# Performance work log

Hardware: AMD Instinct MI355X
Metric: run time of the kernel (lower is better)

Reference implementation:

```python
import jax, jax.numpy as jnp
import numpy as np

B, L = 16, 128
E, A = 34, 36          # num_events, num_arguments
V, D, H = 30000, 300, 256


def setup_inputs() -> dict:
    key = jax.random.key(0)
    ks = jax.random.split(key, 14)
    s = 0.08
    n = lambda k, shape: jax.random.normal(k, shape, jnp.float32) * s
    return {
        "input_ids": jax.random.randint(ks[0], (B, L), 0, V),
        "emb": n(ks[1], (V, D)),
        "Wih_f": n(ks[2], (4 * H, D)), "Whh_f": n(ks[3], (4 * H, H)),
        "bih_f": n(ks[4], (4 * H,)), "bhh_f": n(ks[5], (4 * H,)),
        "Wih_b": n(ks[6], (4 * H, D)), "Whh_b": n(ks[7], (4 * H, H)),
        "bih_b": n(ks[8], (4 * H,)), "bhh_b": n(ks[9], (4 * H,)),
        "We": n(ks[10], (E, 2 * H + E - 1)), "be": n(ks[11], (E,)),
        "Wa": n(ks[12], (A, 4 * H + A - 1 + E - 1)), "ba": n(ks[13], (A,)),
    }


def _lstm(x, Wih, Whh, bih, bhh):
    # x: [L, B, D] -> outputs [L, B, H]; PyTorch gate order i, f, g, o
    Bsz = x.shape[1]
    Hh = Whh.shape[1]
    b = bih + bhh

    def step(carry, xt):
        h, c = carry
        z = xt @ Wih.T + h @ Whh.T + b
        i, f, g, o = jnp.split(z, 4, axis=-1)
        c = jax.nn.sigmoid(f) * c + jax.nn.sigmoid(i) * jnp.tanh(g)
        h = jax.nn.sigmoid(o) * jnp.tanh(c)
        return (h, c), h

    h0 = jnp.zeros((Bsz, Hh), x.dtype)
    _, hs = jax.lax.scan(step, (h0, h0), x)
    return hs


def _forward(input_ids, emb, Wih_f, Whh_f, bih_f, bhh_f, Wih_b, Whh_b, bih_b, bhh_b, We, be, Wa, ba):
    Bsz, Ll = input_ids.shape
    x = emb[input_ids]                       # [B, L, D]
    xt = jnp.transpose(x, (1, 0, 2))         # [L, B, D]
    hf = _lstm(xt, Wih_f, Whh_f, bih_f, bhh_f)
    hb = _lstm(xt[::-1], Wih_b, Whh_b, bih_b, bhh_b)[::-1]
    hs = jnp.concatenate([hf, hb], axis=-1)  # [L, B, 2H]
    hidden = jnp.transpose(hs, (1, 0, 2))    # [B, L, 2H]

    ev_ids = jnp.arange(E - 1)
    ar_ids = jnp.arange(A - 1)
    g_trg0 = jnp.zeros((Bsz, E - 1), jnp.int32)
    g_trg_arg0 = jnp.zeros((Bsz, Ll, E - 1), jnp.int32)
    g_arg0 = jnp.zeros((Bsz, Ll, A - 1), jnp.int32)

    def step(carry, ht):                     # ht: [B, 2H] at position i
        g_trg, g_trg_arg, g_arg = carry
        ev_in = jnp.concatenate([ht, g_trg.astype(ht.dtype)], axis=1)
        ev_logit = ev_in @ We.T + be                       # [B, E]
        ev_pred = jnp.argmax(ev_logit, axis=-1)            # [B]
        trig = jnp.broadcast_to(ht[:, None, :], (Bsz, Ll, ht.shape[-1]))
        arg_in = jnp.concatenate(
            [hidden, trig, g_arg.astype(ht.dtype), g_trg_arg.astype(ht.dtype)], axis=2)
        arg_logits = arg_in @ Wa.T + ba                    # [B, L, A]
        arg_pred = jnp.argmax(arg_logits, axis=-1)         # [B, L]

        has_ev = ev_pred > 0
        # update_g_trg: g_trg[b, ev_pred[b]-1] = 1 where ev_pred>0
        g_trg = jnp.where(has_ev[:, None] & (ev_ids[None, :] == (ev_pred - 1)[:, None]), 1, g_trg)
        # update_g_trg_arg: column ev_pred-1 set to 1 where arg_pred>0
        cond_ta = (has_ev[:, None, None] & (arg_pred > 0)[:, :, None]
                   & (ev_ids[None, None, :] == (ev_pred - 1)[:, None, None]))
        g_trg_arg = jnp.where(cond_ta, 1, g_trg_arg)
        # update_g_arg: g_arg[b, j, arg_pred[b,j]-1] = 1 where ev_pred>0 and arg_pred>0
        cond_a = (has_ev[:, None, None] & (arg_pred > 0)[:, :, None]
                  & (ar_ids[None, None, :] == (arg_pred - 1)[:, :, None]))
        g_arg = jnp.where(cond_a, 1, g_arg)
        return (g_trg, g_trg_arg, g_arg), (ev_logit, arg_logits)

    _, (ev_all, arg_all) = jax.lax.scan(step, (g_trg0, g_trg_arg0, g_arg0), hs)
    event_logits = jnp.transpose(ev_all, (1, 0, 2))        # [B, L, E]
    arguments_logits = jnp.transpose(arg_all, (1, 0, 2, 3))  # [B, L, L, A]
    return event_logits, arguments_logits


def reference(input_ids, emb, Wih_f, Whh_f, bih_f, bhh_f, Wih_b, Whh_b, bih_b, bhh_b, We, be, Wa, ba):
    return _forward(input_ids, emb, Wih_f, Whh_f, bih_f, bhh_f,
                    Wih_b, Whh_b, bih_b, bhh_b, We, be, Wa, ba)
```

## Files before the change

### kernel.cpp

```cpp
#include <hip/hip_runtime.h>
#include <math.h>

#define B_  16
#define L_  128
#define E_  34
#define A_  36
#define D_  300
#define H_  256
#define KP_ 320
#define G4_ 1024
#define KC_ 512
#define NCAT_ 128
#define WAS_ 1092
#define WES_ 545

#define O_XH     0u
#define O_XL     327680u
#define O_WH_F   655360u
#define O_WH_B   819200u
#define O_WL_F   983040u
#define O_WL_B   1146880u
#define O_HX     1310720u
#define O_BSUM_F 1343488u
#define O_BSUM_B 1344512u
#define O_ZPRE   1345536u
#define O_HIDDEN 5539840u
#define O_WCAT   6588416u
#define O_BVEC   6653952u
#define O_P      6654080u
#define O_EVTAG  6916224u

#define HIX(k) ((k) + (((k) >> 5) << 2))

#define BARRIER_LGKM() asm volatile("s_waitcnt lgkmcnt(0)\n\ts_barrier" ::: "memory")

typedef short bf16x8 __attribute__((ext_vector_type(8)));
typedef float f32x4  __attribute__((ext_vector_type(4)));

__device__ __forceinline__ float fsig(float x) {
    return __builtin_amdgcn_rcpf(1.0f + __expf(-x));
}
__device__ __forceinline__ float ftanh(float x) {
    float e = __expf(-2.0f * fabsf(x));
    float t = (1.0f - e) * __builtin_amdgcn_rcpf(1.0f + e);
    return copysignf(t, x);
}
__device__ __forceinline__ unsigned short f2bf(float f) {
    unsigned u = __float_as_uint(f);
    return (unsigned short)((u + 0x7fffu + ((u >> 16) & 1u)) >> 16);
}
__device__ __forceinline__ float bf2f(unsigned short h) {
    return __uint_as_float(((unsigned)h) << 16);
}

__global__ void k_prep(const int* __restrict__ ids, const float* __restrict__ emb,
                       const float* __restrict__ Wih_f,
                       const float* __restrict__ bih_f, const float* __restrict__ bhh_f,
                       const float* __restrict__ Wih_b,
                       const float* __restrict__ bih_b, const float* __restrict__ bhh_b,
                       const float* __restrict__ We, const float* __restrict__ be,
                       const float* __restrict__ Wa, const float* __restrict__ ba,
                       float* __restrict__ ws) {
    const int N0 = 2048 * KP_;
    const int N1 = 2 * G4_ * KP_;
    const int N3 = 2 * 1024;
    const int N4 = 65536;
    const int N5 = 128;
    const int total = N0 + N1 + N3 + N4 + N5;
    unsigned short* xh = (unsigned short*)(ws + O_XH);
    unsigned short* xl = (unsigned short*)(ws + O_XL);
    for (int idx = blockIdx.x * blockDim.x + threadIdx.x; idx < total;
         idx += gridDim.x * blockDim.x) {
        int i = idx;
        if (i < N0) {
            int m = i / KP_, d = i - m * KP_;
            int t = m >> 4, b = m & 15;
            int id = ids[b * L_ + t];
            float f = (d < D_) ? emb[(size_t)id * D_ + d] : 0.0f;
            unsigned short h = f2bf(f);
            xh[i] = h;
            xl[i] = f2bf(f - bf2f(h));
            continue;
        }
        i -= N0;
        if (i < N1) {
            int dir = i / (G4_ * KP_), rem = i % (G4_ * KP_);
            int r = rem / KP_, k = rem - r * KP_;
            const float* Wih = dir ? Wih_b : Wih_f;
            unsigned short* wh = (unsigned short*)(ws + (dir ? O_WH_B : O_WH_F));
            unsigned short* wl = (unsigned short*)(ws + (dir ? O_WL_B : O_WL_F));
            float f = (k < D_) ? Wih[r * D_ + k] : 0.0f;
            unsigned short h = f2bf(f);
            wh[rem] = h;
            wl[rem] = f2bf(f - bf2f(h));
            continue;
        }
        i -= N1;
        if (i < N3) {
            int dir = i / 1024, r = i % 1024;
            ws[(dir ? O_BSUM_B : O_BSUM_F) + r] =
                (dir ? bih_b[r] + bhh_b[r] : bih_f[r] + bhh_f[r]);
            continue;
        }
        i -= N3;
        if (i < N4) {
            int k = i >> 7, n = i & 127;
            float v = 0.0f;
            if (n < 36)               v = Wa[n * WAS_ + k];
            else if (n < 72)          v = Wa[(n - 36) * WAS_ + KC_ + k];
            else if (n < 106)         v = We[(n - 72) * WES_ + k];
            ws[O_WCAT + i] = v;
            continue;
        }
        i -= N4;
        {
            float v = 0.0f;
            if (i < 36)               v = ba[i];
            else if (i >= 72 && i < 106) v = be[i - 72];
            ws[O_BVEC + i] = v;
        }
    }
}

__global__ __launch_bounds__(256) void k_gemm1(float* __restrict__ ws) {
    __shared__ unsigned short Ah[128][40];
    __shared__ unsigned short Al[128][40];
    __shared__ unsigned short Bh[128][40];
    __shared__ unsigned short Bl[128][40];
    int dir = blockIdx.z;
    int m0 = blockIdx.y * 128;
    int n0 = blockIdx.x * 128;
    int tid = threadIdx.x;
    const unsigned short* xh = (const unsigned short*)(ws + O_XH);
    const unsigned short* xl = (const unsigned short*)(ws + O_XL);
    const unsigned short* wh = (const unsigned short*)(ws + (dir ? O_WH_B : O_WH_F));
    const unsigned short* wl = (const unsigned short*)(ws + (dir ? O_WL_B : O_WL_F));
    const float* bsv = ws + (dir ? O_BSUM_B : O_BSUM_F);

    int w = tid >> 6, lane = tid & 63;
    int wr = w >> 1, wc = w & 1;
    int lr = lane & 15, lk = lane >> 4;

    int sr = tid >> 1, sh = tid & 1;
    int gm = m0 + sr;
    int tt = gm >> 4, bb2 = gm & 15;
    int srow = dir ? (((L_ - 1 - tt) << 4) | bb2) : gm;
    size_t aoff = (size_t)srow * KP_ + sh * 16;
    size_t boff = (size_t)(n0 + sr) * KP_ + sh * 16;
    int swb = sr * 80 + sh * 32;

    f32x4 acc[4][4] = {};
    for (int k0 = 0; k0 < KP_; k0 += 32) {
        float4 vah0 = *(const float4*)(xh + aoff + k0);
        float4 vah1 = *(const float4*)(xh + aoff + k0 + 8);
        float4 val0 = *(const float4*)(xl + aoff + k0);
        float4 val1 = *(const float4*)(xl + aoff + k0 + 8);
        float4 vbh0 = *(const float4*)(wh + boff + k0);
        float4 vbh1 = *(const float4*)(wh + boff + k0 + 8);
        float4 vbl0 = *(const float4*)(wl + boff + k0);
        float4 vbl1 = *(const float4*)(wl + boff + k0 + 8);
        *(float4*)((char*)&Ah[0][0] + swb) = vah0;
        *(float4*)((char*)&Ah[0][0] + swb + 16) = vah1;
        *(float4*)((char*)&Al[0][0] + swb) = val0;
        *(float4*)((char*)&Al[0][0] + swb + 16) = val1;
        *(float4*)((char*)&Bh[0][0] + swb) = vbh0;
        *(float4*)((char*)&Bh[0][0] + swb + 16) = vbh1;
        *(float4*)((char*)&Bl[0][0] + swb) = vbl0;
        *(float4*)((char*)&Bl[0][0] + swb + 16) = vbl1;
        __syncthreads();
        bf16x8 afh[4], afl[4], bfh[4], bfl[4];
#pragma unroll
        for (int mi = 0; mi < 4; mi++) {
            int rb = (wr * 64 + mi * 16 + lr) * 80 + lk * 16;
            afh[mi] = *(const bf16x8*)((const char*)&Ah[0][0] + rb);
            afl[mi] = *(const bf16x8*)((const char*)&Al[0][0] + rb);
        }
#pragma unroll
        for (int ni = 0; ni < 4; ni++) {
            int rb = (wc * 64 + ni * 16 + lr) * 80 + lk * 16;
            bfh[ni] = *(const bf16x8*)((const char*)&Bh[0][0] + rb);
            bfl[ni] = *(const bf16x8*)((const char*)&Bl[0][0] + rb);
        }
#pragma unroll
        for (int mi = 0; mi < 4; mi++)
#pragma unroll
            for (int ni = 0; ni < 4; ni++) {
                acc[mi][ni] = __builtin_amdgcn_mfma_f32_16x16x32_bf16(
                    afh[mi], bfh[ni], acc[mi][ni], 0, 0, 0);
                acc[mi][ni] = __builtin_amdgcn_mfma_f32_16x16x32_bf16(
                    afh[mi], bfl[ni], acc[mi][ni], 0, 0, 0);
                acc[mi][ni] = __builtin_amdgcn_mfma_f32_16x16x32_bf16(
                    afl[mi], bfh[ni], acc[mi][ni], 0, 0, 0);
            }
        __syncthreads();
    }
    float* zp = ws + O_ZPRE + (size_t)dir * 2048 * G4_;
    int crow = (lane >> 4) * 4;
#pragma unroll
    for (int ni = 0; ni < 4; ni++) {
        int n = n0 + wc * 64 + ni * 16 + lr;
        float bias = bsv[n];
#pragma unroll
        for (int mi = 0; mi < 4; mi++) {
            int mb = m0 + wr * 64 + mi * 16 + crow;
#pragma unroll
            for (int j = 0; j < 4; j++)
                zp[(size_t)(mb + j) * G4_ + n] = acc[mi][ni][j] + bias;
        }
    }
}

__global__ __launch_bounds__(512, 2) void k_lstm(float* __restrict__ ws,
                                                 const float* __restrict__ Whh_f,
                                                 const float* __restrict__ Whh_b) {
    int phys = blockIdx.x;
    int g    = phys >> 5;
    int cb   = phys & 31;
    int b    = cb & 15;
    int dir  = cb >> 4;
    int tid  = threadIdx.x;
    int rg   = tid >> 3;
    int kc   = tid & 7;

    const float* Whh  = dir ? Whh_b : Whh_f;
    const float* zpre = ws + O_ZPRE + (size_t)dir * 2048 * G4_;
    float* hid = ws + O_HIDDEN;
    unsigned long long* hx64 = (unsigned long long*)(ws + O_HX);

    __shared__ float h_sh[HIX(255) + 1 + 4];
    __shared__ float zbuf[256];

    int lr0  = rg << 2;
    int ggr0 = (lr0 >> 6) * 256 + g * 64 + (lr0 & 63);
    float4 w[4][8];
#pragma unroll
    for (int i = 0; i < 4; i++) {
        const float* wr = Whh + (size_t)(ggr0 + i) * H_ + (kc << 5);
#pragma unroll
        for (int c = 0; c < 8; c++) w[i][c] = *(const float4*)(wr + (c << 2));
    }
    for (int k = tid; k < HIX(255) + 1 + 4; k += 512) h_sh[k] = 0.0f;
    float c_state = 0.0f;
    float4 zv = make_float4(0.f, 0.f, 0.f, 0.f);
    if (kc == 0) zv = *(const float4*)(zpre + (size_t)(0 * B_ + b) * G4_ + ggr0);
    __syncthreads();

    for (int s = 0; s < L_; s++) {
        float4 zn = make_float4(0.f, 0.f, 0.f, 0.f);
        if (kc == 0 && s + 1 < L_)
            zn = *(const float4*)(zpre + (size_t)((s + 1) * B_ + b) * G4_ + ggr0);
        float a0 = 0.f, a1 = 0.f, a2 = 0.f, a3 = 0.f;
        const float* hp = &h_sh[kc * 36];
#pragma unroll
        for (int c = 0; c < 8; c++) {
            float4 hv = *(const float4*)(hp + (c << 2));
            a0 = fmaf(w[0][c].x, hv.x, a0); a0 = fmaf(w[0][c].y, hv.y, a0);
            a0 = fmaf(w[0][c].z, hv.z, a0); a0 = fmaf(w[0][c].w, hv.w, a0);
            a1 = fmaf(w[1][c].x, hv.x, a1); a1 = fmaf(w[1][c].y, hv.y, a1);
            a1 = fmaf(w[1][c].z, hv.z, a1); a1 = fmaf(w[1][c].w, hv.w, a1);
            a2 = fmaf(w[2][c].x, hv.x, a2); a2 = fmaf(w[2][c].y, hv.y, a2);
            a2 = fmaf(w[2][c].z, hv.z, a2); a2 = fmaf(w[2][c].w, hv.w, a2);
            a3 = fmaf(w[3][c].x, hv.x, a3); a3 = fmaf(w[3][c].y, hv.y, a3);
            a3 = fmaf(w[3][c].w, hv.w, a3); a3 = fmaf(w[3][c].z, hv.z, a3);
        }
#pragma unroll
        for (int m = 1; m < 8; m <<= 1) {
            a0 += __shfl_xor(a0, m); a1 += __shfl_xor(a1, m);
            a2 += __shfl_xor(a2, m); a3 += __shfl_xor(a3, m);
        }
        if (kc == 0) {
            float4 z4;
            z4.x = a0 + zv.x; z4.y = a1 + zv.y; z4.z = a2 + zv.z; z4.w = a3 + zv.w;
            *(float4*)&zbuf[lr0] = z4;
        }
        zv = zn;
        BARRIER_LGKM();
        int par = (s + 1) & 1;
        if (tid < 64) {
            float fi = fsig(zbuf[tid]);
            float ff = fsig(zbuf[tid + 64]);
            float gg = ftanh(zbuf[tid + 128]);
            float fo = fsig(zbuf[tid + 192]);
            c_state = ff * c_state + fi * gg;
            float h = fo * ftanh(c_state);
            int hr = g * 64 + tid;
            h_sh[HIX(hr)] = h;
            int t_orig = dir ? (L_ - 1 - s) : s;
            hid[(size_t)(t_orig * B_ + b) * KC_ + dir * H_ + hr] = h;
            if (s + 1 < L_) {
                unsigned long long pk =
                    ((unsigned long long)(unsigned)(s + 1) << 32) | (unsigned)__float_as_uint(h);
                __hip_atomic_store(&hx64[(par << 13) + (phys << 6) + tid], pk,
                                   __ATOMIC_RELAXED, __HIP_MEMORY_SCOPE_AGENT);
            }
        }
        if (tid >= 64 && tid < 256 && s + 1 < L_) {
            int which = tid >> 6;
            int sg = (g + which) & 3;
            int sb = cb | (sg << 5);
            int u  = tid & 63;
            const unsigned long long* wp = &hx64[(par << 13) + (sb << 6) + u];
            unsigned long long v;
            int cnt = 0;
            do {
                v = __hip_atomic_load(wp, __ATOMIC_RELAXED, __HIP_MEMORY_SCOPE_AGENT);
            } while ((int)(v >> 32) < s + 1 && ++cnt < (1 << 20));
            h_sh[HIX(sg * 64 + u)] = __uint_as_float((unsigned)v);
        }
        BARRIER_LGKM();
    }
}

__global__ __launch_bounds__(256) void k_gemm2(float* __restrict__ ws) {
    __shared__ float As[16][64];
    __shared__ float Bs[16][64];
    int m0 = blockIdx.y * 64;
    int n0 = blockIdx.x * 64;
    int tid = threadIdx.x;
    const float* Ap = ws + O_HIDDEN;
    const float* Bp = ws + O_WCAT;
    const float* bv = ws + O_BVEC;
    float acc[4][4] = {};
    int a_m = tid >> 2, a_k = (tid & 3) << 2;
    int b_k = tid >> 4, b_n = (tid & 15) << 2;
    int ty = tid >> 4, tx = tid & 15;
    const float* arow = Ap + (size_t)(m0 + a_m) * KC_;
    for (int k0 = 0; k0 < KC_; k0 += 16) {
        float4 av = *(const float4*)(arow + k0 + a_k);
        float4 bvv = *(const float4*)(Bp + (size_t)(k0 + b_k) * NCAT_ + n0 + b_n);
        As[a_k + 0][a_m] = av.x; As[a_k + 1][a_m] = av.y;
        As[a_k + 2][a_m] = av.z; As[a_k + 3][a_m] = av.w;
        *(float4*)&Bs[b_k][b_n] = bvv;
        __syncthreads();
#pragma unroll
        for (int kk = 0; kk < 16; kk++) {
            float4 a4 = *(const float4*)&As[kk][ty * 4];
            float4 b4 = *(const float4*)&Bs[kk][tx * 4];
            acc[0][0] = fmaf(a4.x, b4.x, acc[0][0]); acc[0][1] = fmaf(a4.x, b4.y, acc[0][1]);
            acc[0][2] = fmaf(a4.x, b4.z, acc[0][2]); acc[0][3] = fmaf(a4.x, b4.w, acc[0][3]);
            acc[1][0] = fmaf(a4.y, b4.x, acc[1][0]); acc[1][1] = fmaf(a4.y, b4.y, acc[1][1]);
            acc[1][2] = fmaf(a4.y, b4.z, acc[1][2]); acc[1][3] = fmaf(a4.y, b4.w, acc[1][3]);
            acc[2][0] = fmaf(a4.z, b4.x, acc[2][0]); acc[2][1] = fmaf(a4.z, b4.y, acc[2][1]);
            acc[2][2] = fmaf(a4.z, b4.z, acc[2][2]); acc[2][3] = fmaf(a4.z, b4.w, acc[2][3]);
            acc[3][0] = fmaf(a4.w, b4.x, acc[3][0]); acc[3][1] = fmaf(a4.w, b4.y, acc[3][1]);
            acc[3][2] = fmaf(a4.w, b4.z, acc[3][2]); acc[3][3] = fmaf(a4.w, b4.w, acc[3][3]);
        }
        __syncthreads();
    }
    float4 bias = *(const float4*)(bv + n0 + tx * 4);
    float* Pp = ws + O_P + (size_t)m0 * NCAT_;
#pragma unroll
    for (int i = 0; i < 4; i++) {
        float4 o;
        o.x = acc[i][0] + bias.x; o.y = acc[i][1] + bias.y;
        o.z = acc[i][2] + bias.z; o.w = acc[i][3] + bias.w;
        *(float4*)(Pp + (size_t)(ty * 4 + i) * NCAT_ + n0 + tx * 4) = o;
    }
}

__global__ __launch_bounds__(1024) void k_dec(const float* __restrict__ We,
                                              const float* __restrict__ Wa,
                                              float* __restrict__ ws, float* __restrict__ out) {
    const float* P = ws + O_P;
    int* evtag = (int*)(ws + O_EVTAG);
    int lane = threadIdx.x & 63;
    if (blockIdx.x == 0) {
        int b = threadIdx.x >> 6;
        float Cg = 0.0f;
        unsigned long long gmask = 0ull;
        float pv = (lane < E_) ? P[(size_t)(0 * B_ + b) * NCAT_ + 72 + lane] : 0.0f;
        float p1 = (lane < E_) ? P[(size_t)(1 * B_ + b) * NCAT_ + 72 + lane] : 0.0f;
        for (int i = 0; i < L_; i++) {
            float p2 = 0.0f;
            if (i + 2 < L_ && lane < E_) p2 = P[(size_t)((i + 2) * B_ + b) * NCAT_ + 72 + lane];
            float v = (lane < E_) ? (pv + Cg) : -INFINITY;
            float mv = v;
            int mi = (lane < E_) ? lane : 0x7fffffff;
#pragma unroll
            for (int off = 32; off; off >>= 1) {
                float ov = __shfl_down(mv, off);
                int oi = __shfl_down(mi, off);
                if (ov > mv || (ov == mv && oi < mi)) { mv = ov; mi = oi; }
            }
            int p = __shfl(mi, 0);
            if (lane == 0)
                __hip_atomic_store(&evtag[b * L_ + i], ((i + 1) << 8) | p,
                                   __ATOMIC_RELAXED, __HIP_MEMORY_SCOPE_AGENT);
            if (lane < E_) out[(size_t)(b * L_ + i) * E_ + lane] = v;
            if (p > 0) {
                unsigned long long bit = 1ull << (p - 1);
                if (!(gmask & bit)) {
                    gmask |= bit;
                    if (lane < E_) Cg += We[lane * WES_ + 2 * H_ + (p - 1)];
                }
            }
            pv = p1; p1 = p2;
        }
    } else {
        int w = ((blockIdx.x - 1) << 4) + (threadIdx.x >> 6);
        int b = w >> 7, j = w & 127;
        float* outa = out + (size_t)B_ * L_ * E_;
        float C = 0.0f;
        if (lane < A_) C = P[(size_t)(j * B_ + b) * NCAT_ + lane];
        unsigned long long ga = 0ull, gta = 0ull;
        float tv = (lane < A_) ? P[(size_t)(0 * B_ + b) * NCAT_ + 36 + lane] : 0.0f;
        float t1 = (lane < A_) ? P[(size_t)(1 * B_ + b) * NCAT_ + 36 + lane] : 0.0f;
        int myv = (int)0x80000000;
        for (int i = 0; i < L_; i++) {
            float t2 = 0.0f;
            if (i + 2 < L_ && lane < A_) t2 = P[(size_t)((i + 2) * B_ + b) * NCAT_ + 36 + lane];
            int w0 = i & ~63;
            if ((i & 63) == 0)
                myv = __hip_atomic_load(&evtag[b * L_ + w0 + lane],
                                        __ATOMIC_RELAXED, __HIP_MEMORY_SCOPE_AGENT);
            int tv_tag = __shfl(myv, i & 63);
            if ((tv_tag >> 8) < i + 1) {
                int cnt = 0;
                do {
                    __builtin_amdgcn_s_sleep(1);
                    myv = __hip_atomic_load(&evtag[b * L_ + w0 + lane],
                                            __ATOMIC_RELAXED, __HIP_MEMORY_SCOPE_AGENT);
                    tv_tag = __shfl(myv, i & 63);
                } while ((tv_tag >> 8) < i + 1 && ++cnt < (1 << 18));
            }
            int ev = tv_tag & 0xff;
            float v = (lane < A_) ? (C + tv) : -INFINITY;
            float mv = v;
            int mi = (lane < A_) ? lane : 0x7fffffff;
#pragma unroll
            for (int off = 32; off; off >>= 1) {
                float ov = __shfl_down(mv, off);
                int oi = __shfl_down(mi, off);
                if (ov > mv || (ov == mv && oi < mi)) { mv = ov; mi = oi; }
            }
            int p = __shfl(mi, 0);
            if (lane < A_) outa[(size_t)((b * L_ + i) * L_ + j) * A_ + lane] = v;
            if (ev > 0 && p > 0) {
                unsigned long long bq = 1ull << (ev - 1);
                if (!(gta & bq)) {
                    gta |= bq;
                    if (lane < A_) C += Wa[lane * WAS_ + 4 * H_ + A_ - 1 + (ev - 1)];
                }
                unsigned long long br = 1ull << (p - 1);
                if (!(ga & br)) {
                    ga |= br;
                    if (lane < A_) C += Wa[lane * WAS_ + 4 * H_ + (p - 1)];
                }
            }
            tv = t1; t1 = t2;
        }
    }
}

extern "C" void kernel_launch(void* const* d_in, const int* in_sizes, int n_in,
                              void* d_out, int out_size, void* d_ws, size_t ws_size,
                              hipStream_t stream) {
    (void)in_sizes; (void)n_in; (void)out_size; (void)ws_size;
    const int*   ids   = (const int*)d_in[0];
    const float* emb   = (const float*)d_in[1];
    const float* Wih_f = (const float*)d_in[2];
    const float* Whh_f = (const float*)d_in[3];
    const float* bih_f = (const float*)d_in[4];
    const float* bhh_f = (const float*)d_in[5];
    const float* Wih_b = (const float*)d_in[6];
    const float* Whh_b = (const float*)d_in[7];
    const float* bih_b = (const float*)d_in[8];
    const float* bhh_b = (const float*)d_in[9];
    const float* We    = (const float*)d_in[10];
    const float* be    = (const float*)d_in[11];
    const float* Wa    = (const float*)d_in[12];
    const float* ba    = (const float*)d_in[13];
    float* out = (float*)d_out;
    float* ws  = (float*)d_ws;

    hipLaunchKernelGGL(k_prep, dim3(2048), dim3(256), 0, stream,
                       ids, emb, Wih_f, bih_f, bhh_f, Wih_b, bih_b, bhh_b,
                       We, be, Wa, ba, ws);
    hipLaunchKernelGGL(k_gemm1, dim3(8, 16, 2), dim3(256), 0, stream, ws);
    hipLaunchKernelGGL(k_lstm, dim3(128), dim3(512), 0, stream, ws, Whh_f, Whh_b);
    hipLaunchKernelGGL(k_gemm2, dim3(2, 32, 1), dim3(256), 0, stream, ws);
    hipLaunchKernelGGL(k_dec, dim3(129), dim3(1024), 0, stream, We, Wa, ws, out);
}
```

Before: 520.2 us.

## Recompute event argmax redundantly per argument wave instead of polling flags

Each argument-decoding wave now runs its own copy of the event-chain argmax recurrence, which is cheap: a 34-wide argmax plus a rare column add per step. This removes the cross-block dependency on the event block's atomic tags and the spin-wait polling with s_sleep. The cost is an extra wave reduction and extra loads of P rows and We columns in every argument wave. The FMA order in the LSTM loop is also restored to the natural z-then-w order.

```diff
diff --git a/kernel.cpp b/kernel.cpp
--- a/kernel.cpp
+++ b/kernel.cpp
@@ -28,7 +28,6 @@
 #define O_WCAT   6588416u
 #define O_BVEC   6653952u
 #define O_P      6654080u
-#define O_EVTAG  6916224u
 
 #define HIX(k) ((k) + (((k) >> 5) << 2))
 
@@ -261,7 +260,7 @@
             a2 = fmaf(w[2][c].x, hv.x, a2); a2 = fmaf(w[2][c].y, hv.y, a2);
             a2 = fmaf(w[2][c].z, hv.z, a2); a2 = fmaf(w[2][c].w, hv.w, a2);
             a3 = fmaf(w[3][c].x, hv.x, a3); a3 = fmaf(w[3][c].y, hv.y, a3);
-            a3 = fmaf(w[3][c].w, hv.w, a3); a3 = fmaf(w[3][c].z, hv.z, a3);
+            a3 = fmaf(w[3][c].z, hv.z, a3); a3 = fmaf(w[3][c].w, hv.w, a3);
         }
 #pragma unroll
         for (int m = 1; m < 8; m <<= 1) {
@@ -362,7 +361,6 @@
                                               const float* __restrict__ Wa,
                                               float* __restrict__ ws, float* __restrict__ out) {
     const float* P = ws + O_P;
-    int* evtag = (int*)(ws + O_EVTAG);
     int lane = threadIdx.x & 63;
     if (blockIdx.x == 0) {
         int b = threadIdx.x >> 6;
@@ -383,9 +381,6 @@
                 if (ov > mv || (ov == mv && oi < mi)) { mv = ov; mi = oi; }
             }
             int p = __shfl(mi, 0);
-            if (lane == 0)
-                __hip_atomic_store(&evtag[b * L_ + i], ((i + 1) << 8) | p,
-                                   __ATOMIC_RELAXED, __HIP_MEMORY_SCOPE_AGENT);
             if (lane < E_) out[(size_t)(b * L_ + i) * E_ + lane] = v;
             if (p > 0) {
                 unsigned long long bit = 1ull << (p - 1);
@@ -403,30 +398,39 @@
         float C = 0.0f;
         if (lane < A_) C = P[(size_t)(j * B_ + b) * NCAT_ + lane];
         unsigned long long ga = 0ull, gta = 0ull;
+        float Cg = 0.0f;
+        unsigned long long gmask = 0ull;
         float tv = (lane < A_) ? P[(size_t)(0 * B_ + b) * NCAT_ + 36 + lane] : 0.0f;
         float t1 = (lane < A_) ? P[(size_t)(1 * B_ + b) * NCAT_ + 36 + lane] : 0.0f;
-        int myv = (int)0x80000000;
+        float pe = (lane < E_) ? P[(size_t)(0 * B_ + b) * NCAT_ + 72 + lane] : 0.0f;
+        float p1 = (lane < E_) ? P[(size_t)(1 * B_ + b) * NCAT_ + 72 + lane] : 0.0f;
         for (int i = 0; i < L_; i++) {
-            float t2 = 0.0f;
-            if (i + 2 < L_ && lane < A_) t2 = P[(size_t)((i + 2) * B_ + b) * NCAT_ + 36 + lane];
-            int w0 = i & ~63;
-            if ((i & 63) == 0)
-                myv = __hip_atomic_load(&evtag[b * L_ + w0 + lane],
-                                        __ATOMIC_RELAXED, __HIP_MEMORY_SCOPE_AGENT);
-            int tv_tag = __shfl(myv, i & 63);
-            if ((tv_tag >> 8) < i + 1) {
-                int cnt = 0;
-                do {
-                    __builtin_amdgcn_s_sleep(1);
-                    myv = __hip_atomic_load(&evtag[b * L_ + w0 + lane],
-                                            __ATOMIC_RELAXED, __HIP_MEMORY_SCOPE_AGENT);
-                    tv_tag = __shfl(myv, i & 63);
-                } while ((tv_tag >> 8) < i + 1 && ++cnt < (1 << 18));
-            }
-            int ev = tv_tag & 0xff;
+            float t2 = 0.0f, p2 = 0.0f;
+            if (i + 2 < L_) {
+                size_t rowb = (size_t)((i + 2) * B_ + b) * NCAT_;
+                if (lane < A_) t2 = P[rowb + 36 + lane];
+                if (lane < E_) p2 = P[rowb + 72 + lane];
+            }
+            float ve = (lane < E_) ? (pe + Cg) : -INFINITY;
+            float mv = ve;
+            int mi = (lane < E_) ? lane : 0x7fffffff;
+#pragma unroll
+            for (int off = 32; off; off >>= 1) {
+                float ov = __shfl_down(mv, off);
+                int oi = __shfl_down(mi, off);
+                if (ov > mv || (ov == mv && oi < mi)) { mv = ov; mi = oi; }
+            }
+            int ev = __shfl(mi, 0);
+            if (ev > 0) {
+                unsigned long long bit = 1ull << (ev - 1);
+                if (!(gmask & bit)) {
+                    gmask |= bit;
+                    if (lane < E_) Cg += We[lane * WES_ + 2 * H_ + (ev - 1)];
+                }
+            }
             float v = (lane < A_) ? (C + tv) : -INFINITY;
-            float mv = v;
-            int mi = (lane < A_) ? lane : 0x7fffffff;
+            mv = v;
+            mi = (lane < A_) ? lane : 0x7fffffff;
 #pragma unroll
             for (int off = 32; off; off >>= 1) {
                 float ov = __shfl_down(mv, off);
@@ -448,6 +452,7 @@
                 }
             }
             tv = t1; t1 = t2;
+            pe = p1; p1 = p2;
         }
     }
 }
```

Result: slower. 558.6 us (+7.4%).
